# Optimization experiments

Measured on AMD Instinct MI355X. Metric: run time of the kernel, lower is better.

The kernel has to match this reference:

```python
import jax, jax.numpy as jnp
import numpy as np

DT = 0.1
THRESH = 10.0

def setup_inputs() -> dict:
    key = jax.random.key(0)
    ks = jax.random.split(key, 6)
    B, S, H, V = 2, 1024, 1024, 50257
    hidden_states = jax.random.normal(ks[0], (B, S, H), dtype=jnp.float32)
    ttu_state = jnp.zeros((B, 3), dtype=jnp.float32)
    W_imp = jax.random.normal(ks[1], (3, H), dtype=jnp.float32) * 0.02
    b_imp = jnp.zeros((3,), dtype=jnp.float32)
    W_lm = jax.random.normal(ks[2], (V, H), dtype=jnp.float32) * 0.02
    W_mod = jax.random.normal(ks[3], (V, 3), dtype=jnp.float32) * 0.02
    # gamma, alpha_c, beta_c, delta, alpha_d, epsilon, alpha_m
    ttu_params = jax.random.uniform(ks[4], (7,), dtype=jnp.float32, minval=0.1, maxval=1.0)
    return {"hidden_states": hidden_states, "ttu_state": ttu_state,
            "W_imp": W_imp, "b_imp": b_imp, "W_lm": W_lm, "W_mod": W_mod,
            "ttu_params": ttu_params}

def _ttu_scan(ttu_state, impulses, ttu_params):
    # impulses: [S, B, 3] (time-major for scan)
    gamma, alpha_c, beta_c, delta, alpha_d, epsilon, alpha_m = ttu_params
    def step(state, imp):
        phi_c, phi_d, phi_m = state[:, 0], state[:, 1], state[:, 2]
        dphi_c = gamma * imp[:, 0] - alpha_c * phi_c - beta_c * phi_c * phi_d
        dphi_d = delta * phi_c ** 2 - alpha_d * phi_d
        dphi_m = epsilon * phi_d - alpha_m * phi_m
        new_c = phi_c + DT * dphi_c
        new_d = phi_d + DT * dphi_d
        new_m = phi_m + DT * dphi_m
        # saturation damping on phi_d
        new_d = jnp.where(jnp.abs(new_d) > THRESH, jnp.float32(0.5), jnp.float32(1.0)) * new_d
        new_state = jnp.stack([new_c, new_d, new_m], axis=1)  # [B, 3]
        return new_state, new_state
    return jax.lax.scan(step, ttu_state, impulses)

def reference(hidden_states, ttu_state, W_imp, b_imp, W_lm, W_mod, ttu_params):
    # impulse projections computed in batch up front: [S, B, 3]
    impulses = jnp.einsum('bsh,dh->sbd', hidden_states, W_imp) + b_imp
    final_state, states = _ttu_scan(ttu_state, impulses, ttu_params)  # states: [S, B, 3]
    # base lm logits + 0.1 * modulation from ttu trajectory
    logits = jnp.einsum('bsh,vh->bsv', hidden_states, W_lm) \
           + 0.1 * jnp.einsum('sbd,vd->bsv', states, W_mod)
    return logits, final_state
```

## Files before the change

### kernel.cpp

```cpp
#include <hip/hip_runtime.h>
#include <hip/hip_bf16.h>

typedef float  f32x4  __attribute__((ext_vector_type(4)));
typedef short  bf16x8 __attribute__((ext_vector_type(8)));
typedef short  bf16x4 __attribute__((ext_vector_type(4)));

typedef const void __attribute__((address_space(1))) gv_t;
typedef void __attribute__((address_space(3))) sv_t;

namespace {

constexpr int B_ = 2;
constexpr int S_ = 1024;
constexpr int H_ = 1024;
constexpr int V_ = 50257;
constexpr int M_ = B_ * S_;
constexpr int VP_ = 50304;
constexpr float DT_ = 0.1f;
constexpr float THRESH_ = 10.0f;

constexpr int BM = 128, BN = 128, BK = 64;
constexpr int LDT = 40;

__device__ __forceinline__ unsigned short f2bf(float f) {
  union { float f; unsigned u; } x;
  x.f = f;
  x.u += 0x7FFFu + ((x.u >> 16) & 1u);
  return (unsigned short)(x.u >> 16);
}

__global__ void ttu_impulse_kernel(const float* __restrict__ hidden,
                                   const float* __restrict__ W_imp,
                                   const float* __restrict__ b_imp,
                                   float* __restrict__ imp) {
  const int m = blockIdx.x;
  const int t = threadIdx.x;
  const float4 hv = reinterpret_cast<const float4*>(hidden + (size_t)m * H_)[t];
  const float4 wv = reinterpret_cast<const float4*>(W_imp)[t];
  float p = hv.x * wv.x + hv.y * wv.y + hv.z * wv.z + hv.w * wv.w;
  #pragma unroll
  for (int off = 32; off; off >>= 1) p += __shfl_down(p, off);
  __shared__ float partial[4];
  if ((t & 63) == 0) partial[t >> 6] = p;
  __syncthreads();
  if (t == 0) {
    const float v = partial[0] + partial[1] + partial[2] + partial[3] + b_imp[0];
    const int b = m >> 10;
    const int s = m & (S_ - 1);
    imp[s * B_ + b] = v;
  }
}

__global__ void ttu_scan_kernel(const float* __restrict__ imp,
                                const float* __restrict__ ttu_state,
                                const float* __restrict__ ttu_params,
                                float* __restrict__ states,
                                float* __restrict__ final_out) {
  __shared__ float imp_s[S_ * B_];
  const int t = threadIdx.x;
  for (int i = t; i < S_ * B_; i += 64) imp_s[i] = imp[i];
  __syncthreads();
  if (t < B_) {
    const float gamma   = ttu_params[0];
    const float alpha_c = ttu_params[1];
    const float beta_c  = ttu_params[2];
    const float delta   = ttu_params[3];
    const float alpha_d = ttu_params[4];
    const float epsilon = ttu_params[5];
    const float alpha_m = ttu_params[6];
    float c = ttu_state[t * 3 + 0];
    float d = ttu_state[t * 3 + 1];
    float m = ttu_state[t * 3 + 2];
    for (int s = 0; s < S_; ++s) {
      const float ii = imp_s[s * B_ + t];
      const float dc = gamma * ii - alpha_c * c - beta_c * c * d;
      const float dd = delta * c * c - alpha_d * d;
      const float dm = epsilon * d - alpha_m * m;
      c = c + DT_ * dc;
      float nd = d + DT_ * dd;
      m = m + DT_ * dm;
      nd = (fabsf(nd) > THRESH_ ? 0.5f : 1.0f) * nd;
      d = nd;
      float* st = states + (size_t)(s * B_ + t) * 3;
      st[0] = c; st[1] = d; st[2] = m;
    }
    final_out[t * 3 + 0] = c;
    final_out[t * 3 + 1] = d;
    final_out[t * 3 + 2] = m;
  }
}

__global__ void cvt_bf16_kernel(const float* __restrict__ src,
                                unsigned short* __restrict__ dst,
                                long n_src, long n_dst) {
  const long stride = (long)gridDim.x * blockDim.x * 8;
  for (long i = ((long)blockIdx.x * blockDim.x + threadIdx.x) * 8; i < n_dst; i += stride) {
    bf16x8 v;
    if (i < n_src) {
      const float4 a = *(const float4*)(src + i);
      const float4 b = *(const float4*)(src + i + 4);
      v[0] = (short)f2bf(a.x); v[1] = (short)f2bf(a.y);
      v[2] = (short)f2bf(a.z); v[3] = (short)f2bf(a.w);
      v[4] = (short)f2bf(b.x); v[5] = (short)f2bf(b.y);
      v[6] = (short)f2bf(b.z); v[7] = (short)f2bf(b.w);
    } else {
      v = (bf16x8){0, 0, 0, 0, 0, 0, 0, 0};
    }
    *(bf16x8*)(dst + i) = v;
  }
}

__global__ __launch_bounds__(256) void ttu_gemm_bf16_kernel(
    const unsigned short* __restrict__ Ab,
    const unsigned short* __restrict__ Bb,
    const float* __restrict__ states,
    const float* __restrict__ Wmod,
    float* __restrict__ out)
{
  __shared__ unsigned short A_s[BM * BK];
  __shared__ unsigned short B_s[BN * BK];
  __shared__ float st_s[BM][3];
  __shared__ float wm_s[BN][3];

  const int t = threadIdx.x;
  const int cpx = gridDim.x >> 3;
  const int bid = (blockIdx.x & 7) * cpx + (blockIdx.x >> 3);
  const int mb = bid & 15;
  const int nb = bid >> 4;
  const int m0 = mb * BM;
  const int n0 = nb * BN;

  if (t < BM) {
    const int m = m0 + t;
    const int b = m >> 10;
    const int s = m & (S_ - 1);
    const float* st = states + (size_t)(s * B_ + b) * 3;
    st_s[t][0] = st[0]; st_s[t][1] = st[1]; st_s[t][2] = st[2];
  } else {
    const int tt = t - BM;
    const int n = n0 + tt;
    const bool ok = n < V_;
    wm_s[tt][0] = ok ? Wmod[n * 3 + 0] : 0.f;
    wm_s[tt][1] = ok ? Wmod[n * 3 + 1] : 0.f;
    wm_s[tt][2] = ok ? Wmod[n * 3 + 2] : 0.f;
  }

  const int lane = t & 63;
  const int wid  = t >> 6;
  const int lr   = lane >> 3;
  const int ch   = lane & 7;
  const int wm   = wid >> 1;
  const int wn   = wid & 1;
  const int lm   = lane & 15;
  const int kg   = lane >> 4;

  f32x4 acc[4][4];
  #pragma unroll
  for (int i = 0; i < 4; ++i)
    #pragma unroll
    for (int j = 0; j < 4; ++j)
      acc[i][j] = (f32x4){0.f, 0.f, 0.f, 0.f};

  const unsigned short* Abase = Ab + (size_t)m0 * H_;
  const unsigned short* Bbase = Bb + (size_t)n0 * H_;

  for (int kt = 0; kt < H_ / BK; ++kt) {
    const int k0 = kt * BK;
    #pragma unroll
    for (int ins = 0; ins < 4; ++ins) {
      const int lrow = wid * 32 + ins * 8 + lr;
      const int sch  = ch ^ (lrow & 7);
      __builtin_amdgcn_global_load_lds(
          (gv_t*)(Abase + (size_t)lrow * H_ + k0 + sch * 8),
          (sv_t*)(A_s + (wid * 32 + ins * 8) * BK), 16, 0, 0);
    }
    #pragma unroll
    for (int ins = 0; ins < 4; ++ins) {
      const int lrow = wid * 32 + ins * 8 + lr;
      const int sch  = ch ^ (lrow & 7);
      __builtin_amdgcn_global_load_lds(
          (gv_t*)(Bbase + (size_t)lrow * H_ + k0 + sch * 8),
          (sv_t*)(B_s + (wid * 32 + ins * 8) * BK), 16, 0, 0);
    }
    __syncthreads();

    bf16x8 af[4][2], bfr[4][2];
    #pragma unroll
    for (int i = 0; i < 4; ++i) {
      const int arow = wm * 64 + i * 16 + lm;
      const int brow = wn * 64 + i * 16 + lm;
      #pragma unroll
      for (int ks = 0; ks < 2; ++ks) {
        af[i][ks]  = *(const bf16x8*)&A_s[arow * BK + (((ks * 4 + kg) ^ (arow & 7)) << 3)];
        bfr[i][ks] = *(const bf16x8*)&B_s[brow * BK + (((ks * 4 + kg) ^ (brow & 7)) << 3)];
      }
    }
    #pragma unroll
    for (int ks = 0; ks < 2; ++ks)
      #pragma unroll
      for (int i = 0; i < 4; ++i)
        #pragma unroll
        for (int j = 0; j < 4; ++j)
          acc[i][j] = __builtin_amdgcn_mfma_f32_16x16x32_bf16(af[i][ks], bfr[j][ks], acc[i][j], 0, 0, 0);
    __syncthreads();
  }

  #pragma unroll
  for (int i = 0; i < 4; ++i) {
    #pragma unroll
    for (int rr = 0; rr < 4; ++rr) {
      const int mloc = wm * 64 + i * 16 + kg * 4 + rr;
      const float s0 = st_s[mloc][0], s1 = st_s[mloc][1], s2 = st_s[mloc][2];
      float* orow = out + (size_t)(m0 + mloc) * V_ + n0;
      #pragma unroll
      for (int j = 0; j < 4; ++j) {
        const int nloc = wn * 64 + j * 16 + lm;
        if (n0 + nloc < V_) {
          const float corr = 0.1f * (s0 * wm_s[nloc][0] + s1 * wm_s[nloc][1] + s2 * wm_s[nloc][2]);
          orow[nloc] = acc[i][j][rr] + corr;
        }
      }
    }
  }
}

__global__ __launch_bounds__(256) void ttu_gemm_kernel(
    const float* __restrict__ Ag, const float* __restrict__ Bg,
    const float* __restrict__ states, const float* __restrict__ Wmod,
    float* __restrict__ out)
{
  __shared__ unsigned short A_s[BM][LDT];
  __shared__ unsigned short B_s[BM][LDT];
  __shared__ float st_s[BM][3];
  __shared__ float wm_s[BM][3];

  const int t   = threadIdx.x;
  const int bid = blockIdx.x;
  const int mb  = bid & 15;
  const int nb  = bid >> 4;
  const int m0  = mb * BM;
  const int n0  = nb * BM;

  if (t < BM) {
    const int m = m0 + t;
    const int b = m >> 10;
    const int s = m & (S_ - 1);
    const float* st = states + (size_t)(s * B_ + b) * 3;
    st_s[t][0] = st[0]; st_s[t][1] = st[1]; st_s[t][2] = st[2];
  } else {
    const int tt = t - BM;
    const int n  = n0 + tt;
    const bool ok = n < V_;
    wm_s[tt][0] = ok ? Wmod[n * 3 + 0] : 0.f;
    wm_s[tt][1] = ok ? Wmod[n * 3 + 1] : 0.f;
    wm_s[tt][2] = ok ? Wmod[n * 3 + 2] : 0.f;
  }

  const int r   = t >> 1;
  const int seg = t & 1;
  const float* arow = Ag + (size_t)(m0 + r) * H_ + seg * 16;
  const int  vrow = n0 + r;
  const bool bok  = vrow < V_;
  const float* brow = Bg + (size_t)(bok ? vrow : 0) * H_ + seg * 16;

  const int lane = t & 63;
  const int wid  = t >> 6;
  const int wm   = wid >> 1;
  const int wn   = wid & 1;
  const int lm   = lane & 15;
  const int kg   = lane >> 4;

  f32x4 acc[4][4];
  #pragma unroll
  for (int i = 0; i < 4; ++i)
    #pragma unroll
    for (int j = 0; j < 4; ++j)
      acc[i][j] = (f32x4){0.f, 0.f, 0.f, 0.f};

  for (int kt = 0; kt < H_ / 32; ++kt) {
    const int k0 = kt * 32;
    const float4 av0 = *(const float4*)(arow + k0 + 0);
    const float4 av1 = *(const float4*)(arow + k0 + 4);
    const float4 av2 = *(const float4*)(arow + k0 + 8);
    const float4 av3 = *(const float4*)(arow + k0 + 12);
    float4 bv0 = {0,0,0,0}, bv1 = {0,0,0,0}, bv2 = {0,0,0,0}, bv3 = {0,0,0,0};
    if (bok) {
      bv0 = *(const float4*)(brow + k0 + 0);
      bv1 = *(const float4*)(brow + k0 + 4);
      bv2 = *(const float4*)(brow + k0 + 8);
      bv3 = *(const float4*)(brow + k0 + 12);
    }
    __syncthreads();
    #define CVT4(v) (bf16x4){(short)f2bf((v).x), (short)f2bf((v).y), (short)f2bf((v).z), (short)f2bf((v).w)}
    *(bf16x4*)&A_s[r][seg * 16 + 0]  = CVT4(av0);
    *(bf16x4*)&A_s[r][seg * 16 + 4]  = CVT4(av1);
    *(bf16x4*)&A_s[r][seg * 16 + 8]  = CVT4(av2);
    *(bf16x4*)&A_s[r][seg * 16 + 12] = CVT4(av3);
    *(bf16x4*)&B_s[r][seg * 16 + 0]  = CVT4(bv0);
    *(bf16x4*)&B_s[r][seg * 16 + 4]  = CVT4(bv1);
    *(bf16x4*)&B_s[r][seg * 16 + 8]  = CVT4(bv2);
    *(bf16x4*)&B_s[r][seg * 16 + 12] = CVT4(bv3);
    #undef CVT4
    __syncthreads();
    bf16x8 af[4], bf[4];
    #pragma unroll
    for (int i = 0; i < 4; ++i) {
      af[i] = *(const bf16x8*)&A_s[wm * 64 + i * 16 + lm][kg * 8];
      bf[i] = *(const bf16x8*)&B_s[wn * 64 + i * 16 + lm][kg * 8];
    }
    #pragma unroll
    for (int i = 0; i < 4; ++i)
      #pragma unroll
      for (int j = 0; j < 4; ++j)
        acc[i][j] = __builtin_amdgcn_mfma_f32_16x16x32_bf16(af[i], bf[j], acc[i][j], 0, 0, 0);
  }

  #pragma unroll
  for (int i = 0; i < 4; ++i) {
    #pragma unroll
    for (int rr = 0; rr < 4; ++rr) {
      const int mloc = wm * 64 + i * 16 + kg * 4 + rr;
      const float s0 = st_s[mloc][0], s1 = st_s[mloc][1], s2 = st_s[mloc][2];
      float* orow = out + (size_t)(m0 + mloc) * V_ + n0;
      #pragma unroll
      for (int j = 0; j < 4; ++j) {
        const int nloc = wn * 64 + j * 16 + lm;
        if (n0 + nloc < V_) {
          const float corr = 0.1f * (s0 * wm_s[nloc][0] + s1 * wm_s[nloc][1] + s2 * wm_s[nloc][2]);
          orow[nloc] = acc[i][j][rr] + corr;
        }
      }
    }
  }
}

}

extern "C" void kernel_launch(void* const* d_in, const int* in_sizes, int n_in,
                              void* d_out, int out_size, void* d_ws, size_t ws_size,
                              hipStream_t stream) {
  const float* hidden     = (const float*)d_in[0];
  const float* ttu_state  = (const float*)d_in[1];
  const float* W_imp      = (const float*)d_in[2];
  const float* b_imp      = (const float*)d_in[3];
  const float* W_lm       = (const float*)d_in[4];
  const float* W_mod      = (const float*)d_in[5];
  const float* ttu_params = (const float*)d_in[6];
  float* out = (float*)d_out;

  float* imp    = (float*)d_ws;
  float* states = imp + S_ * B_;

  const size_t need = 32768 + (size_t)M_ * H_ * 2 + (size_t)VP_ * H_ * 2;
  const int grid = ((VP_ / BN) * (M_ / BM));

  ttu_impulse_kernel<<<M_, 256, 0, stream>>>(hidden, W_imp, b_imp, imp);
  ttu_scan_kernel<<<1, 64, 0, stream>>>(imp, ttu_state, ttu_params, states,
                                        out + (size_t)B_ * S_ * V_);

  if (ws_size >= need) {
    unsigned short* hid_bf = (unsigned short*)((char*)d_ws + 32768);
    unsigned short* wlm_bf = hid_bf + (size_t)M_ * H_;
    cvt_bf16_kernel<<<2048, 256, 0, stream>>>(hidden, hid_bf,
                                              (long)M_ * H_, (long)M_ * H_);
    cvt_bf16_kernel<<<4096, 256, 0, stream>>>(W_lm, wlm_bf,
                                              (long)V_ * H_, (long)VP_ * H_);
    ttu_gemm_bf16_kernel<<<grid, 256, 0, stream>>>(hid_bf, wlm_bf, states, W_mod, out);
  } else {
    ttu_gemm_kernel<<<grid, 256, 0, stream>>>(hidden, W_lm, states, W_mod, out);
  }
}
```

Before: 589.0 us.

## Double-buffer LDS in bf16 GEMM and fuse hidden bf16 conversion into impulse kernel

The bf16 MFMA GEMM now uses two LDS buffers and issues the async global-to-LDS loads for tile k+1 before computing on tile k, so each K iteration needs one barrier instead of two. This is meant to hide global load latency behind the MFMA work. Separately, the conversion of hidden states to bf16 moves into the impulse-projection kernel, which removes one launch and one extra read of the hidden states. The cost is double the LDS per block (64 KB), which may cut occupancy. In the fallback path the bf16 hidden buffer is written at the start of the workspace, on top of the impulse and state buffers.

```diff
diff --git a/kernel.cpp b/kernel.cpp
--- a/kernel.cpp
+++ b/kernel.cpp
@@ -20,7 +20,7 @@
 constexpr float THRESH_ = 10.0f;
 
 constexpr int BM = 128, BN = 128, BK = 64;
-constexpr int LDT = 40;
+constexpr int NT = H_ / BK;
 
 __device__ __forceinline__ unsigned short f2bf(float f) {
   union { float f; unsigned u; } x;
@@ -29,14 +29,19 @@
   return (unsigned short)(x.u >> 16);
 }
 
-__global__ void ttu_impulse_kernel(const float* __restrict__ hidden,
-                                   const float* __restrict__ W_imp,
-                                   const float* __restrict__ b_imp,
-                                   float* __restrict__ imp) {
+__global__ void cvt_hidden_impulse_kernel(const float* __restrict__ hidden,
+                                          const float* __restrict__ W_imp,
+                                          const float* __restrict__ b_imp,
+                                          unsigned short* __restrict__ hid_bf,
+                                          float* __restrict__ imp) {
   const int m = blockIdx.x;
   const int t = threadIdx.x;
   const float4 hv = reinterpret_cast<const float4*>(hidden + (size_t)m * H_)[t];
   const float4 wv = reinterpret_cast<const float4*>(W_imp)[t];
+  bf16x4 o;
+  o[0] = (short)f2bf(hv.x); o[1] = (short)f2bf(hv.y);
+  o[2] = (short)f2bf(hv.z); o[3] = (short)f2bf(hv.w);
+  *(bf16x4*)(hid_bf + (size_t)m * H_ + t * 4) = o;
   float p = hv.x * wv.x + hv.y * wv.y + hv.z * wv.z + hv.w * wv.w;
   #pragma unroll
   for (int off = 32; off; off >>= 1) p += __shfl_down(p, off);
@@ -110,15 +115,14 @@
   }
 }
 
-__global__ __launch_bounds__(256) void ttu_gemm_bf16_kernel(
+__global__ __launch_bounds__(256) void ttu_gemm_bf16_db_kernel(
     const unsigned short* __restrict__ Ab,
     const unsigned short* __restrict__ Bb,
     const float* __restrict__ states,
     const float* __restrict__ Wmod,
     float* __restrict__ out)
 {
-  __shared__ unsigned short A_s[BM * BK];
-  __shared__ unsigned short B_s[BN * BK];
+  __shared__ unsigned short AB_s[2][2][BM * BK];
   __shared__ float st_s[BM][3];
   __shared__ float wm_s[BN][3];
 
@@ -154,35 +158,47 @@
   const int lm   = lane & 15;
   const int kg   = lane >> 4;
 
-  f32x4 acc[4][4];
-  #pragma unroll
-  for (int i = 0; i < 4; ++i)
-    #pragma unroll
-    for (int j = 0; j < 4; ++j)
-      acc[i][j] = (f32x4){0.f, 0.f, 0.f, 0.f};
-
   const unsigned short* Abase = Ab + (size_t)m0 * H_;
   const unsigned short* Bbase = Bb + (size_t)n0 * H_;
 
-  for (int kt = 0; kt < H_ / BK; ++kt) {
+  const int r0 = wid * 32;
+  auto STAGE = [&](unsigned short* As, unsigned short* Bs, int kt) {
     const int k0 = kt * BK;
     #pragma unroll
     for (int ins = 0; ins < 4; ++ins) {
-      const int lrow = wid * 32 + ins * 8 + lr;
+      const int lrow = r0 + ins * 8 + lr;
       const int sch  = ch ^ (lrow & 7);
       __builtin_amdgcn_global_load_lds(
           (gv_t*)(Abase + (size_t)lrow * H_ + k0 + sch * 8),
-          (sv_t*)(A_s + (wid * 32 + ins * 8) * BK), 16, 0, 0);
+          (sv_t*)(As + (r0 + ins * 8) * BK), 16, 0, 0);
     }
     #pragma unroll
     for (int ins = 0; ins < 4; ++ins) {
-      const int lrow = wid * 32 + ins * 8 + lr;
+      const int lrow = r0 + ins * 8 + lr;
       const int sch  = ch ^ (lrow & 7);
       __builtin_amdgcn_global_load_lds(
           (gv_t*)(Bbase + (size_t)lrow * H_ + k0 + sch * 8),
-          (sv_t*)(B_s + (wid * 32 + ins * 8) * BK), 16, 0, 0);
-    }
-    __syncthreads();
+          (sv_t*)(Bs + (r0 + ins * 8) * BK), 16, 0, 0);
+    }
+  };
+
+  f32x4 acc[4][4];
+  #pragma unroll
+  for (int i = 0; i < 4; ++i)
+    #pragma unroll
+    for (int j = 0; j < 4; ++j)
+      acc[i][j] = (f32x4){0.f, 0.f, 0.f, 0.f};
+
+  unsigned short* Ac = &AB_s[0][0][0];
+  unsigned short* Bc = &AB_s[0][1][0];
+  unsigned short* An = &AB_s[1][0][0];
+  unsigned short* Bn = &AB_s[1][1][0];
+
+  STAGE(Ac, Bc, 0);
+  __syncthreads();
+
+  for (int kt = 0; kt < NT; ++kt) {
+    if (kt + 1 < NT) STAGE(An, Bn, kt + 1);
 
     bf16x8 af[4][2], bfr[4][2];
     #pragma unroll
@@ -191,8 +207,8 @@
       const int brow = wn * 64 + i * 16 + lm;
       #pragma unroll
       for (int ks = 0; ks < 2; ++ks) {
-        af[i][ks]  = *(const bf16x8*)&A_s[arow * BK + (((ks * 4 + kg) ^ (arow & 7)) << 3)];
-        bfr[i][ks] = *(const bf16x8*)&B_s[brow * BK + (((ks * 4 + kg) ^ (brow & 7)) << 3)];
+        af[i][ks]  = *(const bf16x8*)&Ac[arow * BK + (((ks * 4 + kg) ^ (arow & 7)) << 3)];
+        bfr[i][ks] = *(const bf16x8*)&Bc[brow * BK + (((ks * 4 + kg) ^ (brow & 7)) << 3)];
       }
     }
     #pragma unroll
@@ -202,7 +218,11 @@
         #pragma unroll
         for (int j = 0; j < 4; ++j)
           acc[i][j] = __builtin_amdgcn_mfma_f32_16x16x32_bf16(af[i][ks], bfr[j][ks], acc[i][j], 0, 0, 0);
+
     __syncthreads();
+    unsigned short* tp;
+    tp = Ac; Ac = An; An = tp;
+    tp = Bc; Bc = Bn; Bn = tp;
   }
 
   #pragma unroll
@@ -229,8 +249,8 @@
     const float* __restrict__ states, const float* __restrict__ Wmod,
     float* __restrict__ out)
 {
-  __shared__ unsigned short A_s[BM][LDT];
-  __shared__ unsigned short B_s[BM][LDT];
+  __shared__ unsigned short A_s[BM][40];
+  __shared__ unsigned short B_s[BM][40];
   __shared__ float st_s[BM][3];
   __shared__ float wm_s[BM][3];
 
@@ -352,21 +372,22 @@
   float* states = imp + S_ * B_;
 
   const size_t need = 32768 + (size_t)M_ * H_ * 2 + (size_t)VP_ * H_ * 2;
-  const int grid = ((VP_ / BN) * (M_ / BM));
-
-  ttu_impulse_kernel<<<M_, 256, 0, stream>>>(hidden, W_imp, b_imp, imp);
-  ttu_scan_kernel<<<1, 64, 0, stream>>>(imp, ttu_state, ttu_params, states,
-                                        out + (size_t)B_ * S_ * V_);
+  const int grid = (VP_ / BN) * (M_ / BM);
 
   if (ws_size >= need) {
     unsigned short* hid_bf = (unsigned short*)((char*)d_ws + 32768);
     unsigned short* wlm_bf = hid_bf + (size_t)M_ * H_;
-    cvt_bf16_kernel<<<2048, 256, 0, stream>>>(hidden, hid_bf,
-                                              (long)M_ * H_, (long)M_ * H_);
+    cvt_hidden_impulse_kernel<<<M_, 256, 0, stream>>>(hidden, W_imp, b_imp, hid_bf, imp);
+    ttu_scan_kernel<<<1, 64, 0, stream>>>(imp, ttu_state, ttu_params, states,
+                                          out + (size_t)B_ * S_ * V_);
     cvt_bf16_kernel<<<4096, 256, 0, stream>>>(W_lm, wlm_bf,
                                               (long)V_ * H_, (long)VP_ * H_);
-    ttu_gemm_bf16_kernel<<<grid, 256, 0, stream>>>(hid_bf, wlm_bf, states, W_mod, out);
+    ttu_gemm_bf16_db_kernel<<<grid, 256, 0, stream>>>(hid_bf, wlm_bf, states, W_mod, out);
   } else {
+    cvt_hidden_impulse_kernel<<<M_, 256, 0, stream>>>(hidden, W_imp, b_imp,
+                                                      (unsigned short*)d_ws , imp);
+    ttu_scan_kernel<<<1, 64, 0, stream>>>(imp, ttu_state, ttu_params, states,
+                                          out + (size_t)B_ * S_ * V_);
     ttu_gemm_kernel<<<grid, 256, 0, stream>>>(hidden, W_lm, states, W_mod, out);
   }
 }
```

Result: faster. 525.2 us (-10.8%).
